# Performance work log

Hardware: AMD Instinct MI355X
Metric: run time of the kernel (lower is better)

Reference implementation:

```python
import jax, jax.numpy as jnp
import numpy as np
from jax import lax

NUM_ITERATIONS = 3
KAPPA = 0.05
DT = 0.25
EPS = 1e-8

# Sobel kernels, normalized by 8, matching the torch buffers. OIHW layout.
_sx = np.array([[-1, 0, 1], [-2, 0, 2], [-1, 0, 1]], dtype=np.float32) / 8.0
_sy = np.array([[-1, -2, -1], [0, 0, 0], [1, 2, 1]], dtype=np.float32) / 8.0
SOBEL_XY = jnp.asarray(np.stack([_sx, _sy])[:, None])  # (2,1,3,3)

_DN = ('NCHW', 'OIHW', 'NCHW')


def _conv(x, w, groups=1):
    return lax.conv_general_dilated(
        x, w, window_strides=(1, 1), padding='SAME',
        dimension_numbers=_DN, feature_group_count=groups)


def setup_inputs() -> dict:
    key = jax.random.key(0)
    image = jax.random.uniform(key, (16, 1, 1024, 1024), dtype=jnp.float32)
    return {"image": image}


def reference(image) -> jnp.ndarray:
    result = image
    for _ in range(NUM_ITERATIONS):
        # (N,2,H,W): ch0 = grad_x, ch1 = grad_y
        grads = _conv(result, SOBEL_XY)
        grad_mag = jnp.sqrt(jnp.sum(grads * grads, axis=1, keepdims=True) + EPS)
        # Perona-Malik g2 conduction: 1 / (1 + (|grad|/kappa)^2)
        c = 1.0 / (1.0 + (grad_mag / KAPPA) ** 2)
        flux = c * grads
        # grouped conv: d/dx on flux_x, d/dy on flux_y, then sum -> divergence
        div_xy = _conv(flux, SOBEL_XY, groups=2)
        divergence = jnp.sum(div_xy, axis=1, keepdims=True)
        result = result + DT * divergence
    return result
```

## Files before the change

kernel.cpp:

```cpp
#include <hip/hip_runtime.h>

#define IMG 1024
#define BH  8

__global__ __launch_bounds__(256, 4)
void pm_sweep(const float* __restrict__ in, float* __restrict__ out) {
    const int tid = threadIdx.x;
    const int c0  = tid << 2;
    const int y0  = blockIdx.x * BH;
    const size_t base = (size_t)blockIdx.y << 20;
    const float* I = in + base;
    float*       O = out + base;

    const bool le = (c0 == 0);
    const bool re = (c0 == IMG - 4);
    const int aC = le ? 0 : c0 - 2;
    const int bC = re ? IMG - 4 : c0 + 2;

    float r0[8], r1[8], r2[8];
    float f1x[6], f1y[6], f2x[6], f2y[6];
    #pragma unroll
    for (int j = 0; j < 8; ++j) { r0[j] = 0.f; r1[j] = 0.f; r2[j] = 0.f; }
    #pragma unroll
    for (int j = 0; j < 6; ++j) { f1x[j] = 0.f; f1y[j] = 0.f; f2x[j] = 0.f; f2y[j] = 0.f; }

    float4 A = make_float4(0.f, 0.f, 0.f, 0.f), B = A;
    if (y0 >= 2) {
        const size_t r = (size_t)(y0 - 2) << 10;
        A = *(const float4*)(I + r + aC);
        B = *(const float4*)(I + r + bC);
    }

    #pragma unroll
    for (int k = 0; k < BH + 4; ++k) {
        const int yld = y0 - 2 + k;

        #pragma unroll
        for (int j = 0; j < 8; ++j) { r2[j] = r1[j]; r1[j] = r0[j]; }
        r0[0] = le ? 0.f : A.x;  r0[1] = le ? 0.f : A.y;
        r0[2] = le ? A.x : A.z;  r0[3] = le ? A.y : A.w;
        r0[4] = re ? B.z : B.x;  r0[5] = re ? B.w : B.y;
        r0[6] = re ? 0.f : B.z;  r0[7] = re ? 0.f : B.w;

        if (k < BH + 3) {
            const int row = yld + 1;
            if (row >= 0 && row < IMG) {
                const size_t r = (size_t)row << 10;
                A = *(const float4*)(I + r + aC);
                B = *(const float4*)(I + r + bC);
            } else { A = make_float4(0.f, 0.f, 0.f, 0.f); B = A; }
        }

        float fNx[6], fNy[6];
        const int yf = yld - 1;
        if (yf >= 0 && yf < IMG) {
            float s[8], d[8];
            #pragma unroll
            for (int j = 0; j < 8; ++j) {
                s[j] = fmaf(2.f, r1[j], r2[j] + r0[j]);
                d[j] = r0[j] - r2[j];
            }
            #pragma unroll
            for (int i = 0; i < 6; ++i) {
                const float GX  = s[i+2] - s[i];
                const float GY  = fmaf(2.f, d[i+1], d[i] + d[i+2]);
                const float m2  = fmaf(GY, GY, GX * GX);
                const float mag = fmaf(m2, 0.015625f, 1e-8f);
                const float den = fmaf(mag, 400.f, 1.f);
                const float c   = __builtin_amdgcn_rcpf(den);
                fNx[i] = c * GX;
                fNy[i] = c * GY;
            }
            if (le) { fNx[0] = 0.f; fNy[0] = 0.f; }
            if (re) { fNx[5] = 0.f; fNy[5] = 0.f; }
        } else {
            #pragma unroll
            for (int i = 0; i < 6; ++i) { fNx[i] = 0.f; fNy[i] = 0.f; }
        }

        if (k >= 4) {
            float S[6], D[6];
            #pragma unroll
            for (int j = 0; j < 6; ++j) {
                S[j] = fmaf(2.f, f1x[j], f2x[j] + fNx[j]);
                D[j] = fNy[j] - f2y[j];
            }
            float o[4];
            #pragma unroll
            for (int i = 0; i < 4; ++i) {
                const float DX = S[i+2] - S[i];
                const float DY = fmaf(2.f, D[i+1], D[i] + D[i+2]);
                o[i] = fmaf(DX + DY, 0.00390625f, r2[i+2]);
            }
            const int yd = yld - 2;
            *(float4*)(O + ((size_t)yd << 10) + c0) = make_float4(o[0], o[1], o[2], o[3]);
        }

        #pragma unroll
        for (int j = 0; j < 6; ++j) {
            f2x[j] = f1x[j]; f2y[j] = f1y[j];
            f1x[j] = fNx[j]; f1y[j] = fNy[j];
        }
    }
}

extern "C" void kernel_launch(void* const* d_in, const int* in_sizes, int n_in,
                              void* d_out, int out_size, void* d_ws, size_t ws_size,
                              hipStream_t stream) {
    const float* img = (const float*)d_in[0];
    float* out = (float*)d_out;
    float* ws  = (float*)d_ws;
    const int N = in_sizes[0] / (IMG * IMG);

    dim3 grid(IMG / BH, N);
    dim3 block(256);
    pm_sweep<<<grid, block, 0, stream>>>(img, out);
    pm_sweep<<<grid, block, 0, stream>>>(out, ws);
    pm_sweep<<<grid, block, 0, stream>>>(ws, out);
}
```

Measured before the change: 169.6 us.

## Fuse three diffusion iterations into one kernel with LDS row ring buffers

Replaces three separate sweep launches with a single kernel that pipelines all three Perona-Malik iterations per row band. Intermediate rows are kept in shared-memory ring buffers, and input rows are brought in with global_load_lds async copies. This removes two full-image global round trips and two launches. In exchange, halo rows are recomputed (a 16-row band needs 12 extra steps), there are two barriers per step, and the band height goes from 8 to 16.

```diff
diff --git a/kernel.cpp b/kernel.cpp
--- a/kernel.cpp
+++ b/kernel.cpp
@@ -1,65 +1,73 @@
 #include <hip/hip_runtime.h>
 
-#define IMG 1024
-#define BH  8
+#define IMG   1024
+#define BH    16
+#define STEPS (BH + 12)
+#define LW    1032
+#define PADL  4
+
+typedef __attribute__((address_space(1))) const void gv_t;
+typedef __attribute__((address_space(3))) void lv_t;
 
 __global__ __launch_bounds__(256, 4)
-void pm_sweep(const float* __restrict__ in, float* __restrict__ out) {
+void pm_fused3(const float* __restrict__ in, float* __restrict__ out) {
+    __shared__ __align__(16) float S[9 * LW];
+
     const int tid = threadIdx.x;
     const int c0  = tid << 2;
-    const int y0  = blockIdx.x * BH;
+    const int Y0  = blockIdx.x * BH;
     const size_t base = (size_t)blockIdx.y << 20;
     const float* I = in + base;
-    float*       O = out + base;
+    float* O = out + base;
+    const bool le = (c0 == 0), re = (c0 == IMG - 4);
 
-    const bool le = (c0 == 0);
-    const bool re = (c0 == IMG - 4);
-    const int aC = le ? 0 : c0 - 2;
-    const int bC = re ? IMG - 4 : c0 + 2;
-
-    float r0[8], r1[8], r2[8];
-    float f1x[6], f1y[6], f2x[6], f2y[6];
-    #pragma unroll
-    for (int j = 0; j < 8; ++j) { r0[j] = 0.f; r1[j] = 0.f; r2[j] = 0.f; }
-    #pragma unroll
-    for (int j = 0; j < 6; ++j) { f1x[j] = 0.f; f1y[j] = 0.f; f2x[j] = 0.f; f2y[j] = 0.f; }
-
-    float4 A = make_float4(0.f, 0.f, 0.f, 0.f), B = A;
-    if (y0 >= 2) {
-        const size_t r = (size_t)(y0 - 2) << 10;
-        A = *(const float4*)(I + r + aC);
-        B = *(const float4*)(I + r + bC);
+    if (tid < 72) {
+        const int r = tid >> 3, j = tid & 7;
+        S[r * LW + ((j < 4) ? j : (1024 + j))] = 0.f;
     }
 
+    int i0 = 0,    i1 = LW,     i2 = 2 * LW;
+    int u0 = 3*LW, u1 = 4 * LW, u2 = 5 * LW;
+    int v0 = 6*LW, v1 = 7 * LW, v2 = 8 * LW;
+
+    const int wb = (tid >> 6) << 8;
+
+    {
+        const int row = Y0 - 6;
+        if (row >= 0)
+            __builtin_amdgcn_global_load_lds((gv_t*)(I + ((size_t)row << 10) + c0),
+                                             (lv_t*)(S + i0 + PADL + wb), 16, 0, 0);
+        else
+            *(float4*)&S[i0 + PADL + c0] = make_float4(0.f, 0.f, 0.f, 0.f);
+    }
+    __syncthreads();
+
+    const int vbw = PADL + c0 - 2;
+
+    float a1x[6],a1y[6],a2x[6],a2y[6];
+    float b1x[6],b1y[6],b2x[6],b2y[6];
+    float c1x[6],c1y[6],c2x[6],c2y[6];
     #pragma unroll
-    for (int k = 0; k < BH + 4; ++k) {
-        const int yld = y0 - 2 + k;
+    for (int j = 0; j < 6; ++j) {
+        a1x[j]=a1y[j]=a2x[j]=a2y[j]=0.f;
+        b1x[j]=b1y[j]=b2x[j]=b2y[j]=0.f;
+        c1x[j]=c1y[j]=c2x[j]=c2y[j]=0.f;
+    }
 
-        #pragma unroll
-        for (int j = 0; j < 8; ++j) { r2[j] = r1[j]; r1[j] = r0[j]; }
-        r0[0] = le ? 0.f : A.x;  r0[1] = le ? 0.f : A.y;
-        r0[2] = le ? A.x : A.z;  r0[3] = le ? A.y : A.w;
-        r0[4] = re ? B.z : B.x;  r0[5] = re ? B.w : B.y;
-        r0[6] = re ? 0.f : B.z;  r0[7] = re ? 0.f : B.w;
+    auto rd8 = [&](int ro, float* w) {
+        float2 t0 = *(const float2*)&S[ro + vbw];
+        float4 t1 = *(const float4*)&S[ro + vbw + 2];
+        float2 t2 = *(const float2*)&S[ro + vbw + 6];
+        w[0]=t0.x; w[1]=t0.y; w[2]=t1.x; w[3]=t1.y;
+        w[4]=t1.z; w[5]=t1.w; w[6]=t2.x; w[7]=t2.y;
+    };
 
-        if (k < BH + 3) {
-            const int row = yld + 1;
-            if (row >= 0 && row < IMG) {
-                const size_t r = (size_t)row << 10;
-                A = *(const float4*)(I + r + aC);
-                B = *(const float4*)(I + r + bC);
-            } else { A = make_float4(0.f, 0.f, 0.f, 0.f); B = A; }
-        }
-
-        float fNx[6], fNy[6];
-        const int yf = yld - 1;
-        if (yf >= 0 && yf < IMG) {
+    auto flux6 = [&](const float* um, const float* uc, const float* up, bool valid,
+                     float* fx, float* fy) {
+        if (valid) {
             float s[8], d[8];
             #pragma unroll
-            for (int j = 0; j < 8; ++j) {
-                s[j] = fmaf(2.f, r1[j], r2[j] + r0[j]);
-                d[j] = r0[j] - r2[j];
-            }
+            for (int j = 0; j < 8; ++j) { s[j]=fmaf(2.f,uc[j],um[j]+up[j]); d[j]=up[j]-um[j]; }
             #pragma unroll
             for (int i = 0; i < 6; ++i) {
                 const float GX  = s[i+2] - s[i];
@@ -68,39 +76,83 @@
                 const float mag = fmaf(m2, 0.015625f, 1e-8f);
                 const float den = fmaf(mag, 400.f, 1.f);
                 const float c   = __builtin_amdgcn_rcpf(den);
-                fNx[i] = c * GX;
-                fNy[i] = c * GY;
+                fx[i] = c * GX; fy[i] = c * GY;
             }
-            if (le) { fNx[0] = 0.f; fNy[0] = 0.f; }
-            if (re) { fNx[5] = 0.f; fNy[5] = 0.f; }
+            if (le) { fx[0]=0.f; fy[0]=0.f; }
+            if (re) { fx[5]=0.f; fy[5]=0.f; }
         } else {
             #pragma unroll
-            for (int i = 0; i < 6; ++i) { fNx[i] = 0.f; fNy[i] = 0.f; }
+            for (int i = 0; i < 6; ++i) { fx[i]=0.f; fy[i]=0.f; }
         }
+    };
 
-        if (k >= 4) {
-            float S[6], D[6];
-            #pragma unroll
-            for (int j = 0; j < 6; ++j) {
-                S[j] = fmaf(2.f, f1x[j], f2x[j] + fNx[j]);
-                D[j] = fNy[j] - f2y[j];
-            }
-            float o[4];
-            #pragma unroll
-            for (int i = 0; i < 4; ++i) {
-                const float DX = S[i+2] - S[i];
-                const float DY = fmaf(2.f, D[i+1], D[i] + D[i+2]);
-                o[i] = fmaf(DX + DY, 0.00390625f, r2[i+2]);
-            }
-            const int yd = yld - 2;
-            *(float4*)(O + ((size_t)yd << 10) + c0) = make_float4(o[0], o[1], o[2], o[3]);
-        }
-
+    auto div4 = [&](const float* f2x_, const float* f1x_, const float* fNx_,
+                    const float* f2y_, const float* f1y_, const float* fNy_,
+                    const float* ctr, bool wr, float* o) {
+        float Sx[6], Dy[6];
         #pragma unroll
         for (int j = 0; j < 6; ++j) {
-            f2x[j] = f1x[j]; f2y[j] = f1y[j];
-            f1x[j] = fNx[j]; f1y[j] = fNy[j];
+            Sx[j] = fmaf(2.f, f1x_[j], f2x_[j] + fNx_[j]);
+            Dy[j] = fNy_[j] - f2y_[j];
         }
+        #pragma unroll
+        for (int i = 0; i < 4; ++i) {
+            const float DX = Sx[i+2] - Sx[i];
+            const float DY = fmaf(2.f, Dy[i+1], Dy[i] + Dy[i+2]);
+            o[i] = wr ? fmaf(DX + DY, 0.00390625f, ctr[i+2]) : 0.f;
+        }
+    };
+
+    #pragma unroll 2
+    for (int k = 0; k < STEPS; ++k) {
+        float um[8], uc[8], up[8];
+        rd8(i2, um); rd8(i1, uc); rd8(i0, up);
+        float aNx[6], aNy[6];
+        const int yf1 = Y0 - 7 + k;
+        flux6(um, uc, up, (unsigned)yf1 < IMG, aNx, aNy);
+        const int L1 = Y0 - 8 + k;
+        float o1[4];
+        div4(a2x,a1x,aNx, a2y,a1y,aNy, um, (k >= 4) && ((unsigned)L1 < IMG), o1);
+        { int t=u2; u2=u1; u1=u0; u0=t; }
+        *(float4*)&S[u0 + PADL + c0] = make_float4(o1[0],o1[1],o1[2],o1[3]);
+        #pragma unroll
+        for (int j=0;j<6;++j){ a2x[j]=a1x[j]; a2y[j]=a1y[j]; a1x[j]=aNx[j]; a1y[j]=aNy[j]; }
+        __syncthreads();
+
+        if (k < STEPS - 1) {
+            { int t=i2; i2=i1; i1=i0; i0=t; }
+            const int row = Y0 - 5 + k;
+            if ((unsigned)row < IMG)
+                __builtin_amdgcn_global_load_lds((gv_t*)(I + ((size_t)row << 10) + c0),
+                                                 (lv_t*)(S + i0 + PADL + wb), 16, 0, 0);
+            else
+                *(float4*)&S[i0 + PADL + c0] = make_float4(0.f, 0.f, 0.f, 0.f);
+        }
+        float vm[8], vc[8], vp[8];
+        rd8(u2, vm); rd8(u1, vc); rd8(u0, vp);
+        float bNx[6], bNy[6];
+        flux6(vm, vc, vp, (unsigned)(L1 - 1) < IMG, bNx, bNy);
+        const int h = L1 - 2;
+        float o2[4];
+        div4(b2x,b1x,bNx, b2y,b1y,bNy, vm, (k >= 8) && ((unsigned)h < IMG), o2);
+        { int t=v2; v2=v1; v1=v0; v0=t; }
+        *(float4*)&S[v0 + PADL + c0] = make_float4(o2[0],o2[1],o2[2],o2[3]);
+        #pragma unroll
+        for (int j=0;j<6;++j){ b2x[j]=b1x[j]; b2y[j]=b1y[j]; b1x[j]=bNx[j]; b1y[j]=bNy[j]; }
+        __syncthreads();
+
+        float wm[8], wc[8], wp[8];
+        rd8(v2, wm); rd8(v1, wc); rd8(v0, wp);
+        float cNx[6], cNy[6];
+        flux6(wm, wc, wp, (unsigned)(h - 1) < IMG, cNx, cNy);
+        float o3[4];
+        div4(c2x,c1x,cNx, c2y,c1y,cNy, wm, true, o3);
+        if (k >= 12) {
+            const int y = Y0 + (k - 12);
+            *(float4*)(O + ((size_t)y << 10) + c0) = make_float4(o3[0],o3[1],o3[2],o3[3]);
+        }
+        #pragma unroll
+        for (int j=0;j<6;++j){ c2x[j]=c1x[j]; c2y[j]=c1y[j]; c1x[j]=cNx[j]; c1y[j]=cNy[j]; }
     }
 }
 
@@ -109,12 +161,9 @@
                               hipStream_t stream) {
     const float* img = (const float*)d_in[0];
     float* out = (float*)d_out;
-    float* ws  = (float*)d_ws;
     const int N = in_sizes[0] / (IMG * IMG);
 
     dim3 grid(IMG / BH, N);
     dim3 block(256);
-    pm_sweep<<<grid, block, 0, stream>>>(img, out);
-    pm_sweep<<<grid, block, 0, stream>>>(out, ws);
-    pm_sweep<<<grid, block, 0, stream>>>(ws, out);
+    pm_fused3<<<grid, block, 0, stream>>>(img, out);
 }
```

New measurement: 236.9 us. +39.7%, slower.
